# Optimization experiments

Measured on AMD Instinct MI355X. Metric: run time of the kernel, lower is better.

The kernel has to match this reference:

```python
import jax, jax.numpy as jnp
import numpy as np

N, DEG, IN_DIM, HID, OUT = 50000, 32, 256, 256, 128

def setup_inputs() -> dict:
    key = jax.random.key(0)
    k1, k2, k3, k4, k5, k6 = jax.random.split(key, 6)
    node_features = jax.random.normal(k1, (N, IN_DIM), dtype=jnp.float32)
    neighbor_idx = jax.random.randint(k2, (N, DEG), 0, N)
    scale1 = 1.0 / np.sqrt(2 * IN_DIM)
    scale2 = 1.0 / np.sqrt(HID)
    W1 = jax.random.normal(k3, (HID, 2 * IN_DIM), dtype=jnp.float32) * scale1
    b1 = jax.random.normal(k4, (HID,), dtype=jnp.float32) * scale1
    W2 = jax.random.normal(k5, (OUT, HID), dtype=jnp.float32) * scale2
    b2 = jax.random.normal(k6, (OUT,), dtype=jnp.float32) * scale2
    return {"node_features": node_features, "neighbor_idx": neighbor_idx,
            "W1": W1, "b1": b1, "W2": W2, "b2": b2}

def reference(node_features, neighbor_idx, W1, b1, W2, b2):
    # Layer 0 (mean aggregator, with neighbors):
    # gather [N, DEG, IN_DIM] neighbor features, mean over DEG
    nbr_mean = jnp.mean(node_features[neighbor_idx], axis=1)  # [N, IN_DIM]
    combined = jnp.concatenate([node_features, nbr_mean], axis=-1)  # [N, 2*IN_DIM]
    h = jax.nn.relu(combined @ W1.T + b1)  # [N, HID]
    # Layer 1: empty neighbor list -> linear_without_neighbors + relu
    out = jax.nn.relu(h @ W2.T + b2)  # [N, OUT]
    return out
```

## Files before the change

kernel.cpp:

```cpp
#include <hip/hip_runtime.h>
#include <stdint.h>

#define N_NODES 50000
#define DEG     32
#define IN_DIM  256
#define K1      512
#define HID     256
#define OUT_DIM 128

#define NCHUNK  4
#define CDIM    64
#define SLICE8  ((size_t)N_NODES * CDIM)
#define GT      16

#define MT     32
#define NTILES ((N_NODES + MT - 1) / MT)
#define GBLK   256
#define CSTR   520
#define HSTR   264

typedef __bf16 bf16x8 __attribute__((ext_vector_type(8)));
typedef float  f32x4  __attribute__((ext_vector_type(4)));
typedef float  f32x2  __attribute__((ext_vector_type(2)));

#define PIN(x) asm volatile("" : "+v"(x))

__device__ __forceinline__ unsigned short f2bf(float f) {
    union { float f; unsigned u; } v; v.f = f;
    unsigned r = v.u + 0x7fffu + ((v.u >> 16) & 1u);
    return (unsigned short)(r >> 16);
}
__device__ __forceinline__ int clampN(int v) {
    return v < 0 ? 0 : (v >= N_NODES ? N_NODES - 1 : v);
}
__device__ __forceinline__ void async_copy16(const void* g, void* l) {
    __builtin_amdgcn_global_load_lds(
        (const __attribute__((address_space(1))) void*)g,
        (__attribute__((address_space(3))) void*)l, 16, 0, 0);
}

#define FEAT_BLKS ((N_NODES + 7) / 8)
__global__ __launch_bounds__(256)
void prep_all(const float* __restrict__ feat,
              const float* __restrict__ W1, const float* __restrict__ W2,
              const int*   __restrict__ nbr,
              unsigned short* __restrict__ featb,
              unsigned char*  __restrict__ featF8,
              unsigned short* __restrict__ W1b, unsigned short* __restrict__ W2b,
              unsigned short* __restrict__ nbr16)
{
    const int t = threadIdx.x;
    if (blockIdx.x < FEAT_BLKS) {
        const int node = blockIdx.x * 8 + (t >> 5);
        const int seg  = t & 31;
        if (node < N_NODES) {
            const float4* src = (const float4*)(feat + (size_t)node * IN_DIM + seg * 8);
            float4 f0 = src[0], f1 = src[1];
            ushort4 o0, o1;
            o0.x = f2bf(f0.x); o0.y = f2bf(f0.y); o0.z = f2bf(f0.z); o0.w = f2bf(f0.w);
            o1.x = f2bf(f1.x); o1.y = f2bf(f1.y); o1.z = f2bf(f1.z); o1.w = f2bf(f1.w);
            unsigned short* db = featb + (size_t)node * IN_DIM + seg * 8;
            *(ushort4*)db       = o0;
            *(ushort4*)(db + 4) = o1;
            int u0 = 0, u1 = 0;
            u0 = __builtin_amdgcn_cvt_pk_fp8_f32(f0.x, f0.y, u0, false);
            u0 = __builtin_amdgcn_cvt_pk_fp8_f32(f0.z, f0.w, u0, true);
            u1 = __builtin_amdgcn_cvt_pk_fp8_f32(f1.x, f1.y, u1, false);
            u1 = __builtin_amdgcn_cvt_pk_fp8_f32(f1.z, f1.w, u1, true);
            const int c   = seg >> 3;
            const int off = (seg & 7) * 8;
            unsigned char* d8 = featF8 + (size_t)c * SLICE8 + (size_t)node * CDIM + off;
            ((int*)d8)[0] = u0;
            ((int*)d8)[1] = u1;
        }
    } else {
        const int bid = blockIdx.x - FEAT_BLKS;
        const int stride = 256 * 256 * 4;
        const int tid4 = (bid * 256 + t) * 4;
        for (int i = tid4; i < HID * K1; i += stride) {
            float4 f = *(const float4*)(W1 + i);
            ushort4 o; o.x = f2bf(f.x); o.y = f2bf(f.y); o.z = f2bf(f.z); o.w = f2bf(f.w);
            *(ushort4*)(W1b + i) = o;
        }
        for (int i = tid4; i < OUT_DIM * HID; i += stride) {
            float4 f = *(const float4*)(W2 + i);
            ushort4 o; o.x = f2bf(f.x); o.y = f2bf(f.y); o.z = f2bf(f.z); o.w = f2bf(f.w);
            *(ushort4*)(W2b + i) = o;
        }
        for (int i = tid4; i < N_NODES * DEG; i += stride) {
            int4 v = *(const int4*)(nbr + i);
            ushort4 o;
            o.x = (unsigned short)clampN(v.x); o.y = (unsigned short)clampN(v.y);
            o.z = (unsigned short)clampN(v.z); o.w = (unsigned short)clampN(v.w);
            *(ushort4*)(nbr16 + i) = o;
        }
    }
}

__global__ __launch_bounds__(256)
void gather_mean_fp8(const unsigned char*  __restrict__ featF8,
                     const unsigned short* __restrict__ nbr16,
                     unsigned short*       __restrict__ meanb)
{
    __shared__ unsigned short sIdx[GT * DEG];
    const int tid  = threadIdx.x;
    const int c    = blockIdx.y;
    const int base = blockIdx.x * GT;

    if (tid < 128) {
        *(ushort4*)(sIdx + tid * 4) =
            *(const ushort4*)(nbr16 + (size_t)base * DEG + tid * 4);
    }
    __syncthreads();

    const unsigned char* slice = featF8 + (size_t)c * SLICE8;
    const int grp = tid >> 4;
    const int ln  = tid & 15;
    const unsigned short* idxr = sIdx + grp * DEG;

    unsigned vv[DEG];
    #pragma unroll
    for (int j = 0; j < DEG; ++j) {
        int nb = idxr[j];
        vv[j] = *(const unsigned*)(slice + (size_t)nb * CDIM + ln * 4);
    }
    float s0 = 0.f, s1 = 0.f, s2 = 0.f, s3 = 0.f;
    #pragma unroll
    for (int j = 0; j < DEG; ++j) {
        f32x2 lo = __builtin_amdgcn_cvt_pk_f32_fp8(vv[j], false);
        f32x2 hi = __builtin_amdgcn_cvt_pk_f32_fp8(vv[j], true);
        s0 += lo[0]; s1 += lo[1]; s2 += hi[0]; s3 += hi[1];
    }
    const float sc = 1.0f / 32.0f;
    ushort4 o;
    o.x = f2bf(s0 * sc); o.y = f2bf(s1 * sc);
    o.z = f2bf(s2 * sc); o.w = f2bf(s3 * sc);
    const int node = base + grp;
    *(ushort4*)(meanb + (size_t)node * IN_DIM + c * CDIM + ln * 4) = o;
}

__global__ __launch_bounds__(512, 2)
void sage_gemm_dbuf(const unsigned short* __restrict__ featb,
                    const unsigned short* __restrict__ meanb,
                    const unsigned short* __restrict__ W1b,
                    const float*          __restrict__ b1,
                    const unsigned short* __restrict__ W2b,
                    const float*          __restrict__ b2,
                    float*                __restrict__ out)
{
    __shared__ __align__(16) unsigned short sC[2][MT * CSTR];
    __shared__ __align__(16) unsigned short sH[MT * HSTR];

    const int tid  = threadIdx.x;
    const int lane = tid & 63;
    const int wave = tid >> 6;
    const int r    = lane & 15;
    const int q    = lane >> 4;

    bf16x8 w1f[2][16];
    #pragma unroll
    for (int nt = 0; nt < 2; ++nt) {
        const size_t nrow = (size_t)(wave * 32 + nt * 16 + r) * K1;
        #pragma unroll
        for (int kk = 0; kk < 16; ++kk) {
            w1f[nt][kk] = *(const bf16x8*)(W1b + nrow + kk * 32 + q * 8);
            PIN(w1f[nt][kk]);
        }
    }
    bf16x8 w2f[8];
    {
        const size_t orow = (size_t)(wave * 16 + r) * HID;
        #pragma unroll
        for (int kk = 0; kk < 8; ++kk) {
            w2f[kk] = *(const bf16x8*)(W2b + orow + kk * 32 + q * 8);
            PIN(w2f[kk]);
        }
    }
    const float bias1a = b1[wave * 32 + r];
    const float bias1b = b1[wave * 32 + 16 + r];
    const float bias2  = b2[wave * 16 + r];

    auto stage = [&](int tile, int buf) {
        const int base = tile * MT;
        #pragma unroll
        for (int j = 0; j < 4; ++j) {
            const int i = wave * 4 + j;
            int node = base + i;
            if (node >= N_NODES) node = N_NODES - 1;
            const unsigned short* g = (lane < 32)
                ? featb + (size_t)node * IN_DIM + lane * 8
                : meanb + (size_t)node * IN_DIM + (lane - 32) * 8;
            async_copy16(g, &sC[buf][i * CSTR]);
        }
    };

    int tile = blockIdx.x;
    if (tile < NTILES) stage(tile, 0);
    int buf = 0;

    for (; tile < NTILES; tile += GBLK) {
        __syncthreads();

        const int nxt = tile + GBLK;
        if (nxt < NTILES) stage(nxt, buf ^ 1);

        {
            f32x4 acc[2][2];
            #pragma unroll
            for (int mt = 0; mt < 2; ++mt)
                #pragma unroll
                for (int nt = 0; nt < 2; ++nt)
                    acc[mt][nt] = (f32x4){0.f, 0.f, 0.f, 0.f};

            #pragma unroll
            for (int kk = 0; kk < 16; ++kk) {
                bf16x8 a0 = *(const bf16x8*)(&sC[buf][r * CSTR + kk * 32 + q * 8]);
                bf16x8 a1 = *(const bf16x8*)(&sC[buf][(16 + r) * CSTR + kk * 32 + q * 8]);
                acc[0][0] = __builtin_amdgcn_mfma_f32_16x16x32_bf16(a0, w1f[0][kk], acc[0][0], 0, 0, 0);
                acc[1][0] = __builtin_amdgcn_mfma_f32_16x16x32_bf16(a1, w1f[0][kk], acc[1][0], 0, 0, 0);
                acc[0][1] = __builtin_amdgcn_mfma_f32_16x16x32_bf16(a0, w1f[1][kk], acc[0][1], 0, 0, 0);
                acc[1][1] = __builtin_amdgcn_mfma_f32_16x16x32_bf16(a1, w1f[1][kk], acc[1][1], 0, 0, 0);
            }
            #pragma unroll
            for (int nt = 0; nt < 2; ++nt) {
                const int n = wave * 32 + nt * 16 + r;
                const float bias = nt ? bias1b : bias1a;
                #pragma unroll
                for (int mt = 0; mt < 2; ++mt)
                    #pragma unroll
                    for (int g = 0; g < 4; ++g) {
                        const int m = mt * 16 + q * 4 + g;
                        float v = acc[mt][nt][g] + bias;
                        sH[m * HSTR + n] = f2bf(v > 0.f ? v : 0.f);
                    }
            }
        }
        __syncthreads();

        {
            f32x4 acc3[2];
            acc3[0] = (f32x4){0.f, 0.f, 0.f, 0.f};
            acc3[1] = (f32x4){0.f, 0.f, 0.f, 0.f};
            #pragma unroll
            for (int kk = 0; kk < 8; ++kk) {
                bf16x8 h0 = *(const bf16x8*)(&sH[r * HSTR + kk * 32 + q * 8]);
                bf16x8 h1 = *(const bf16x8*)(&sH[(16 + r) * HSTR + kk * 32 + q * 8]);
                acc3[0] = __builtin_amdgcn_mfma_f32_16x16x32_bf16(h0, w2f[kk], acc3[0], 0, 0, 0);
                acc3[1] = __builtin_amdgcn_mfma_f32_16x16x32_bf16(h1, w2f[kk], acc3[1], 0, 0, 0);
            }
            const int base = tile * MT;
            const int o = wave * 16 + r;
            #pragma unroll
            for (int mt = 0; mt < 2; ++mt)
                #pragma unroll
                for (int g = 0; g < 4; ++g) {
                    const int m = mt * 16 + q * 4 + g;
                    const int node = base + m;
                    if (node < N_NODES) {
                        float v = acc3[mt][g] + bias2;
                        out[(size_t)node * OUT_DIM + o] = v > 0.f ? v : 0.f;
                    }
                }
        }
        buf ^= 1;
    }
}

__global__ __launch_bounds__(256)
void sage_naive(const float* __restrict__ feat, const int* __restrict__ nbr,
                const float* __restrict__ W1, const float* __restrict__ b1,
                const float* __restrict__ W2, const float* __restrict__ b2,
                float* __restrict__ out) {
    __shared__ float comb[K1];
    __shared__ float h[HID];
    const int node = blockIdx.x;
    const int t = threadIdx.x;
    comb[t] = feat[(size_t)node * IN_DIM + t];
    float acc = 0.f;
    for (int d = 0; d < DEG; ++d) {
        int nb = clampN(nbr[node * DEG + d]);
        acc += feat[(size_t)nb * IN_DIM + t];
    }
    comb[IN_DIM + t] = acc * (1.0f / 32.0f);
    __syncthreads();
    float s = b1[t];
    for (int k = 0; k < K1; ++k) s += comb[k] * W1[(size_t)t * K1 + k];
    h[t] = s > 0.f ? s : 0.f;
    __syncthreads();
    if (t < OUT_DIM) {
        float s2 = b2[t];
        for (int k = 0; k < HID; ++k) s2 += h[k] * W2[(size_t)t * HID + k];
        out[(size_t)node * OUT_DIM + t] = s2 > 0.f ? s2 : 0.f;
    }
}

extern "C" void kernel_launch(void* const* d_in, const int* in_sizes, int n_in,
                              void* d_out, int out_size, void* d_ws, size_t ws_size,
                              hipStream_t stream) {
    const float* feat = (const float*)d_in[0];
    const int*   nbr  = (const int*)d_in[1];
    const float* W1   = (const float*)d_in[2];
    const float* b1   = (const float*)d_in[3];
    const float* W2   = (const float*)d_in[4];
    const float* b2   = (const float*)d_in[5];
    float* out = (float*)d_out;

    const size_t feat_elems = (size_t)N_NODES * IN_DIM;
    const size_t w1_elems   = (size_t)HID * K1;
    const size_t w2_elems   = (size_t)OUT_DIM * HID;
    const size_t mean_elems = (size_t)N_NODES * IN_DIM;
    const size_t idx_elems  = (size_t)N_NODES * DEG;
    const size_t u16_elems  = feat_elems + w1_elems + w2_elems + mean_elems + idx_elems;
    const size_t need = u16_elems * sizeof(unsigned short)
                      + (size_t)NCHUNK * SLICE8;

    if (ws_size >= need) {
        unsigned short* featb  = (unsigned short*)d_ws;
        unsigned short* W1b    = featb + feat_elems;
        unsigned short* W2b    = W1b + w1_elems;
        unsigned short* meanb  = W2b + w2_elems;
        unsigned short* nbr16  = meanb + mean_elems;
        unsigned char*  featF8 = (unsigned char*)(nbr16 + idx_elems);

        prep_all<<<FEAT_BLKS + 256, 256, 0, stream>>>(feat, W1, W2, nbr,
                                                      featb, featF8, W1b, W2b, nbr16);
        gather_mean_fp8<<<dim3(N_NODES / GT, NCHUNK), 256, 0, stream>>>(featF8, nbr16, meanb);
        sage_gemm_dbuf<<<GBLK, 512, 0, stream>>>(featb, meanb, W1b, b1, W2b, b2, out);
    } else {
        sage_naive<<<N_NODES, 256, 0, stream>>>(feat, nbr, W1, b1, W2, b2, out);
    }
}
```

Baseline: 174.3 us.

## Software-pipeline the fused GEMM across tiles and widen gather loads

The fused two-layer GEMM kernel double-buffers the hidden tile in shared memory, so the second GEMM for the previous tile runs after the first GEMM of the current tile. This removes one barrier per tile. The MFMA operands are swapped so accumulators come out transposed, which allows vectorized ushort4 hidden writes and float4 output stores in place of scalar stores. The gather kernel now uses 128 threads, each loading 8 fp8 bytes per neighbor instead of 4, which halves the number of load instructions at the cost of more registers per thread.

```diff
diff --git a/kernel.cpp b/kernel.cpp
--- a/kernel.cpp
+++ b/kernel.cpp
@@ -97,7 +97,7 @@
     }
 }
 
-__global__ __launch_bounds__(256)
+__global__ __launch_bounds__(128)
 void gather_mean_fp8(const unsigned char*  __restrict__ featF8,
                      const unsigned short* __restrict__ nbr16,
                      unsigned short*       __restrict__ meanb)
@@ -107,40 +107,46 @@
     const int c    = blockIdx.y;
     const int base = blockIdx.x * GT;
 
-    if (tid < 128) {
-        *(ushort4*)(sIdx + tid * 4) =
-            *(const ushort4*)(nbr16 + (size_t)base * DEG + tid * 4);
-    }
+    *(ushort4*)(sIdx + tid * 4) =
+        *(const ushort4*)(nbr16 + (size_t)base * DEG + tid * 4);
     __syncthreads();
 
     const unsigned char* slice = featF8 + (size_t)c * SLICE8;
-    const int grp = tid >> 4;
-    const int ln  = tid & 15;
+    const int grp = tid >> 3;
+    const int ln  = tid & 7;
     const unsigned short* idxr = sIdx + grp * DEG;
 
-    unsigned vv[DEG];
+    uint2 vv[DEG];
     #pragma unroll
     for (int j = 0; j < DEG; ++j) {
         int nb = idxr[j];
-        vv[j] = *(const unsigned*)(slice + (size_t)nb * CDIM + ln * 4);
-    }
-    float s0 = 0.f, s1 = 0.f, s2 = 0.f, s3 = 0.f;
+        vv[j] = *(const uint2*)(slice + (size_t)nb * CDIM + ln * 8);
+    }
+    float s[8];
+    #pragma unroll
+    for (int k = 0; k < 8; ++k) s[k] = 0.f;
     #pragma unroll
     for (int j = 0; j < DEG; ++j) {
-        f32x2 lo = __builtin_amdgcn_cvt_pk_f32_fp8(vv[j], false);
-        f32x2 hi = __builtin_amdgcn_cvt_pk_f32_fp8(vv[j], true);
-        s0 += lo[0]; s1 += lo[1]; s2 += hi[0]; s3 += hi[1];
+        f32x2 a = __builtin_amdgcn_cvt_pk_f32_fp8(vv[j].x, false);
+        f32x2 b = __builtin_amdgcn_cvt_pk_f32_fp8(vv[j].x, true);
+        f32x2 d = __builtin_amdgcn_cvt_pk_f32_fp8(vv[j].y, false);
+        f32x2 e = __builtin_amdgcn_cvt_pk_f32_fp8(vv[j].y, true);
+        s[0] += a[0]; s[1] += a[1]; s[2] += b[0]; s[3] += b[1];
+        s[4] += d[0]; s[5] += d[1]; s[6] += e[0]; s[7] += e[1];
     }
     const float sc = 1.0f / 32.0f;
-    ushort4 o;
-    o.x = f2bf(s0 * sc); o.y = f2bf(s1 * sc);
-    o.z = f2bf(s2 * sc); o.w = f2bf(s3 * sc);
-    const int node = base + grp;
-    *(ushort4*)(meanb + (size_t)node * IN_DIM + c * CDIM + ln * 4) = o;
+    ushort4 o0, o1;
+    o0.x = f2bf(s[0] * sc); o0.y = f2bf(s[1] * sc);
+    o0.z = f2bf(s[2] * sc); o0.w = f2bf(s[3] * sc);
+    o1.x = f2bf(s[4] * sc); o1.y = f2bf(s[5] * sc);
+    o1.z = f2bf(s[6] * sc); o1.w = f2bf(s[7] * sc);
+    unsigned short* dst = meanb + (size_t)(base + grp) * IN_DIM + c * CDIM + ln * 8;
+    *(ushort4*)dst       = o0;
+    *(ushort4*)(dst + 4) = o1;
 }
 
 __global__ __launch_bounds__(512, 2)
-void sage_gemm_dbuf(const unsigned short* __restrict__ featb,
+void sage_gemm_pipe(const unsigned short* __restrict__ featb,
                     const unsigned short* __restrict__ meanb,
                     const unsigned short* __restrict__ W1b,
                     const float*          __restrict__ b1,
@@ -149,7 +155,7 @@
                     float*                __restrict__ out)
 {
     __shared__ __align__(16) unsigned short sC[2][MT * CSTR];
-    __shared__ __align__(16) unsigned short sH[MT * HSTR];
+    __shared__ __align__(16) unsigned short sH[2][MT * HSTR];
 
     const int tid  = threadIdx.x;
     const int lane = tid & 63;
@@ -176,16 +182,16 @@
             PIN(w2f[kk]);
         }
     }
-    const float bias1a = b1[wave * 32 + r];
-    const float bias1b = b1[wave * 32 + 16 + r];
-    const float bias2  = b2[wave * 16 + r];
+    const float4 bias1v0 = *(const float4*)(b1 + wave * 32 + q * 4);
+    const float4 bias1v1 = *(const float4*)(b1 + wave * 32 + 16 + q * 4);
+    const float4 bias2v  = *(const float4*)(b2 + wave * 16 + q * 4);
 
     auto stage = [&](int tile, int buf) {
-        const int base = tile * MT;
+        const int tbase = tile * MT;
         #pragma unroll
         for (int j = 0; j < 4; ++j) {
             const int i = wave * 4 + j;
-            int node = base + i;
+            int node = tbase + i;
             if (node >= N_NODES) node = N_NODES - 1;
             const unsigned short* g = (lane < 32)
                 ? featb + (size_t)node * IN_DIM + lane * 8
@@ -194,76 +200,81 @@
         }
     };
 
+    auto phase2 = [&](int cbuf, int hbuf) {
+        f32x4 acc[2][2];
+        #pragma unroll
+        for (int mt = 0; mt < 2; ++mt)
+            #pragma unroll
+            for (int nt = 0; nt < 2; ++nt)
+                acc[mt][nt] = (f32x4){0.f, 0.f, 0.f, 0.f};
+        #pragma unroll
+        for (int kk = 0; kk < 16; ++kk) {
+            bf16x8 a0 = *(const bf16x8*)(&sC[cbuf][r * CSTR + kk * 32 + q * 8]);
+            bf16x8 a1 = *(const bf16x8*)(&sC[cbuf][(16 + r) * CSTR + kk * 32 + q * 8]);
+            acc[0][0] = __builtin_amdgcn_mfma_f32_16x16x32_bf16(w1f[0][kk], a0, acc[0][0], 0, 0, 0);
+            acc[1][0] = __builtin_amdgcn_mfma_f32_16x16x32_bf16(w1f[0][kk], a1, acc[1][0], 0, 0, 0);
+            acc[0][1] = __builtin_amdgcn_mfma_f32_16x16x32_bf16(w1f[1][kk], a0, acc[0][1], 0, 0, 0);
+            acc[1][1] = __builtin_amdgcn_mfma_f32_16x16x32_bf16(w1f[1][kk], a1, acc[1][1], 0, 0, 0);
+        }
+        #pragma unroll
+        for (int nt = 0; nt < 2; ++nt) {
+            const float4 bias = nt ? bias1v1 : bias1v0;
+            #pragma unroll
+            for (int mt = 0; mt < 2; ++mt) {
+                float v0 = acc[mt][nt][0] + bias.x;
+                float v1 = acc[mt][nt][1] + bias.y;
+                float v2 = acc[mt][nt][2] + bias.z;
+                float v3 = acc[mt][nt][3] + bias.w;
+                ushort4 o;
+                o.x = f2bf(v0 > 0.f ? v0 : 0.f);
+                o.y = f2bf(v1 > 0.f ? v1 : 0.f);
+                o.z = f2bf(v2 > 0.f ? v2 : 0.f);
+                o.w = f2bf(v3 > 0.f ? v3 : 0.f);
+                *(ushort4*)(&sH[hbuf][(mt * 16 + r) * HSTR + wave * 32 + nt * 16 + q * 4]) = o;
+            }
+        }
+    };
+
+    auto phase3 = [&](int hbuf, int pbase) {
+        f32x4 acc3[2];
+        acc3[0] = (f32x4){0.f, 0.f, 0.f, 0.f};
+        acc3[1] = (f32x4){0.f, 0.f, 0.f, 0.f};
+        #pragma unroll
+        for (int kk = 0; kk < 8; ++kk) {
+            bf16x8 h0 = *(const bf16x8*)(&sH[hbuf][r * HSTR + kk * 32 + q * 8]);
+            bf16x8 h1 = *(const bf16x8*)(&sH[hbuf][(16 + r) * HSTR + kk * 32 + q * 8]);
+            acc3[0] = __builtin_amdgcn_mfma_f32_16x16x32_bf16(w2f[kk], h0, acc3[0], 0, 0, 0);
+            acc3[1] = __builtin_amdgcn_mfma_f32_16x16x32_bf16(w2f[kk], h1, acc3[1], 0, 0, 0);
+        }
+        #pragma unroll
+        for (int mt = 0; mt < 2; ++mt) {
+            const int node = pbase + mt * 16 + r;
+            if (node < N_NODES) {
+                float4 v;
+                v.x = acc3[mt][0] + bias2v.x; v.x = v.x > 0.f ? v.x : 0.f;
+                v.y = acc3[mt][1] + bias2v.y; v.y = v.y > 0.f ? v.y : 0.f;
+                v.z = acc3[mt][2] + bias2v.z; v.z = v.z > 0.f ? v.z : 0.f;
+                v.w = acc3[mt][3] + bias2v.w; v.w = v.w > 0.f ? v.w : 0.f;
+                *(float4*)(out + (size_t)node * OUT_DIM + wave * 16 + q * 4) = v;
+            }
+        }
+    };
+
     int tile = blockIdx.x;
+    int buf = 0, hb = 0;
+    int prev_base = -1;
     if (tile < NTILES) stage(tile, 0);
-    int buf = 0;
 
     for (; tile < NTILES; tile += GBLK) {
         __syncthreads();
-
-        const int nxt = tile + GBLK;
-        if (nxt < NTILES) stage(nxt, buf ^ 1);
-
-        {
-            f32x4 acc[2][2];
-            #pragma unroll
-            for (int mt = 0; mt < 2; ++mt)
-                #pragma unroll
-                for (int nt = 0; nt < 2; ++nt)
-                    acc[mt][nt] = (f32x4){0.f, 0.f, 0.f, 0.f};
-
-            #pragma unroll
-            for (int kk = 0; kk < 16; ++kk) {
-                bf16x8 a0 = *(const bf16x8*)(&sC[buf][r * CSTR + kk * 32 + q * 8]);
-                bf16x8 a1 = *(const bf16x8*)(&sC[buf][(16 + r) * CSTR + kk * 32 + q * 8]);
-                acc[0][0] = __builtin_amdgcn_mfma_f32_16x16x32_bf16(a0, w1f[0][kk], acc[0][0], 0, 0, 0);
-                acc[1][0] = __builtin_amdgcn_mfma_f32_16x16x32_bf16(a1, w1f[0][kk], acc[1][0], 0, 0, 0);
-                acc[0][1] = __builtin_amdgcn_mfma_f32_16x16x32_bf16(a0, w1f[1][kk], acc[0][1], 0, 0, 0);
-                acc[1][1] = __builtin_amdgcn_mfma_f32_16x16x32_bf16(a1, w1f[1][kk], acc[1][1], 0, 0, 0);
-            }
-            #pragma unroll
-            for (int nt = 0; nt < 2; ++nt) {
-                const int n = wave * 32 + nt * 16 + r;
-                const float bias = nt ? bias1b : bias1a;
-                #pragma unroll
-                for (int mt = 0; mt < 2; ++mt)
-                    #pragma unroll
-                    for (int g = 0; g < 4; ++g) {
-                        const int m = mt * 16 + q * 4 + g;
-                        float v = acc[mt][nt][g] + bias;
-                        sH[m * HSTR + n] = f2bf(v > 0.f ? v : 0.f);
-                    }
-            }
-        }
-        __syncthreads();
-
-        {
-            f32x4 acc3[2];
-            acc3[0] = (f32x4){0.f, 0.f, 0.f, 0.f};
-            acc3[1] = (f32x4){0.f, 0.f, 0.f, 0.f};
-            #pragma unroll
-            for (int kk = 0; kk < 8; ++kk) {
-                bf16x8 h0 = *(const bf16x8*)(&sH[r * HSTR + kk * 32 + q * 8]);
-                bf16x8 h1 = *(const bf16x8*)(&sH[(16 + r) * HSTR + kk * 32 + q * 8]);
-                acc3[0] = __builtin_amdgcn_mfma_f32_16x16x32_bf16(h0, w2f[kk], acc3[0], 0, 0, 0);
-                acc3[1] = __builtin_amdgcn_mfma_f32_16x16x32_bf16(h1, w2f[kk], acc3[1], 0, 0, 0);
-            }
-            const int base = tile * MT;
-            const int o = wave * 16 + r;
-            #pragma unroll
-            for (int mt = 0; mt < 2; ++mt)
-                #pragma unroll
-                for (int g = 0; g < 4; ++g) {
-                    const int m = mt * 16 + q * 4 + g;
-                    const int node = base + m;
-                    if (node < N_NODES) {
-                        float v = acc3[mt][g] + bias2;
-                        out[(size_t)node * OUT_DIM + o] = v > 0.f ? v : 0.f;
-                    }
-                }
-        }
-        buf ^= 1;
-    }
+        if (tile + GBLK < NTILES) stage(tile + GBLK, buf ^ 1);
+        phase2(buf, hb);
+        if (prev_base >= 0) phase3(hb ^ 1, prev_base);
+        prev_base = tile * MT;
+        buf ^= 1; hb ^= 1;
+    }
+    __syncthreads();
+    if (prev_base >= 0) phase3(hb ^ 1, prev_base);
 }
 
 __global__ __launch_bounds__(256)
@@ -324,8 +335,8 @@
 
         prep_all<<<FEAT_BLKS + 256, 256, 0, stream>>>(feat, W1, W2, nbr,
                                                       featb, featF8, W1b, W2b, nbr16);
-        gather_mean_fp8<<<dim3(N_NODES / GT, NCHUNK), 256, 0, stream>>>(featF8, nbr16, meanb);
-        sage_gemm_dbuf<<<GBLK, 512, 0, stream>>>(featb, meanb, W1b, b1, W2b, b2, out);
+        gather_mean_fp8<<<dim3(N_NODES / GT, NCHUNK), 128, 0, stream>>>(featF8, nbr16, meanb);
+        sage_gemm_pipe<<<GBLK, 512, 0, stream>>>(featb, meanb, W1b, b1, W2b, b2, out);
     } else {
         sage_naive<<<N_NODES, 256, 0, stream>>>(feat, nbr, W1, b1, W2, b2, out);
     }
```

Result: no change. 177.2 us (+1.7%).
